# Kernel tuning notes

Measured on AMD Instinct MI355X. Metric: run time of the kernel, lower is better.

The kernel has to match this reference:

```python
import jax, jax.numpy as jnp
import numpy as np

B, V, D = 1024, 50000, 300
EPS = 1e-7


def setup_inputs() -> dict:
    key = jax.random.key(0)
    k1, k2 = jax.random.split(key)
    # soft multi-hot label mask over the vocab (torch code multiplies floats)
    labels = jax.random.uniform(k1, (B, V), dtype=jnp.float32)
    # pretrained word2vec-style embedding table
    weight = jax.random.normal(k2, (V, D), dtype=jnp.float32)
    return {"labels": labels, "weight": weight}


def reference(labels, weight):
    # torch: mul(weight, labels[:, :, None]).sum(1)  ==  labels @ weight
    attr = jnp.einsum('bv,vd->bd', labels, weight)  # (B, D)
    # L2 normalize: attr / (sqrt(sum(attr^2, 1)) + 1e-7)
    norm = jnp.sqrt(jnp.sum(attr * attr, axis=1, keepdims=True))
    return attr / (norm + EPS)
```

## Files before the change

kernel.cpp:

```cpp
#include <hip/hip_runtime.h>
#include <hip/hip_bf16.h>
#include <math.h>

typedef __bf16 bf16;
typedef bf16 bf16x8 __attribute__((ext_vector_type(8)));
typedef float f32x4 __attribute__((ext_vector_type(4)));

constexpr int Mdim = 1024;
constexpr int Kdim = 50000;
constexpr int Ndim = 300;
constexpr int NP   = 320;

constexpr int BM = 64, BN = 320, BK = 64;
constexpr int BKP = 72;
constexpr int MT = Mdim / BM;

__device__ __forceinline__ bf16x8 bzero8() {
    bf16x8 v;
#pragma unroll
    for (int e = 0; e < 8; ++e) v[e] = (bf16)0.0f;
    return v;
}

constexpr int TK = 64;
constexpr int TS = 301;
__global__ __launch_bounds__(256) void transpose_w(const float* __restrict__ W,
                                                   bf16* __restrict__ Wt)
{
    __shared__ bf16 tile[TK * TS];
    const int k0 = blockIdx.x * TK;
    const int t  = threadIdx.x;

    for (int c = t; c < 64 * 75; c += 256) {
        const int kk = c / 75;
        const int ch = c % 75;
        const int k  = k0 + kk;
        float4 v = make_float4(0.f, 0.f, 0.f, 0.f);
        if (k < Kdim) v = *(const float4*)(W + (size_t)k * Ndim + ch * 4);
        bf16* p = &tile[kk * TS + ch * 4];
        p[0] = (bf16)v.x; p[1] = (bf16)v.y; p[2] = (bf16)v.z; p[3] = (bf16)v.w;
    }
    __syncthreads();
    for (int c = t; c < NP * 8; c += 256) {
        const int n  = c >> 3;
        const int ch = c & 7;
        const int k  = k0 + ch * 8;
        if (k + 8 <= Kdim) {
            bf16x8 v = bzero8();
            if (n < Ndim) {
#pragma unroll
                for (int j = 0; j < 8; ++j) v[j] = tile[(ch * 8 + j) * TS + n];
            }
            *(bf16x8*)(Wt + (size_t)n * Kdim + k) = v;
        }
    }
}

template<int SPLIT, int SEGLEN, bool ATOMIC>
__global__ __launch_bounds__(512, 4) void gemm_kernel(const float* __restrict__ A,
                                                      const bf16* __restrict__ Wt,
                                                      float* __restrict__ out)
{
    __shared__ bf16 As[BM * BKP];
    __shared__ bf16 Bs[BN * BKP];

    const int bx   = blockIdx.x;
    const int mt   = bx & (MT - 1);
    const int ks   = bx >> 4;
    const int m0   = mt * BM;
    const int kbeg = ks * SEGLEN;
    const int kend = min(kbeg + SEGLEN, Kdim);

    const int t    = threadIdx.x;
    const int lane = t & 63;
    const int wave = t >> 6;
    const int wm   = wave >> 2;
    const int wn   = wave & 3;
    const int lm   = lane & 15;
    const int lq   = lane >> 4;

    const int arow = t >> 3;
    const int acol = (t & 7) * 8;
    const float* aptr = A + (size_t)(m0 + arow) * Kdim;

    float4 af[2];
    bf16x8 bfr[5];

    auto load_tiles = [&](int k0) {
        const int k = k0 + acol;
        if (k + 8 <= kend) {
            af[0] = *(const float4*)(aptr + k);
            af[1] = *(const float4*)(aptr + k + 4);
        } else {
            af[0] = make_float4(0.f, 0.f, 0.f, 0.f);
            af[1] = make_float4(0.f, 0.f, 0.f, 0.f);
        }
#pragma unroll
        for (int i = 0; i < 5; ++i) {
            const int c = t + 512 * i;
            const int brow = c >> 3;
            const int bcol = (c & 7) * 8;
            const int kk = k0 + bcol;
            bfr[i] = (kk + 8 <= kend) ? *(const bf16x8*)(Wt + (size_t)brow * Kdim + kk)
                                      : bzero8();
        }
    };
    auto store_tiles = [&]() {
        bf16x8 v;
        v[0]=(bf16)af[0].x; v[1]=(bf16)af[0].y; v[2]=(bf16)af[0].z; v[3]=(bf16)af[0].w;
        v[4]=(bf16)af[1].x; v[5]=(bf16)af[1].y; v[6]=(bf16)af[1].z; v[7]=(bf16)af[1].w;
        *(bf16x8*)(&As[arow * BKP + acol]) = v;
#pragma unroll
        for (int i = 0; i < 5; ++i) {
            const int c = t + 512 * i;
            const int brow = c >> 3;
            const int bcol = (c & 7) * 8;
            *(bf16x8*)(&Bs[brow * BKP + bcol]) = bfr[i];
        }
    };

    f32x4 acc[2][5] = {};

    load_tiles(kbeg);
    for (int k0 = kbeg; k0 < kend; k0 += BK) {
        store_tiles();
        __syncthreads();
        if (k0 + BK < kend) load_tiles(k0 + BK);
#pragma unroll
        for (int s = 0; s < 2; ++s) {
            bf16x8 a[2], b[5];
#pragma unroll
            for (int i = 0; i < 2; ++i)
                a[i] = *(const bf16x8*)(&As[(wm * 32 + i * 16 + lm) * BKP + s * 32 + lq * 8]);
#pragma unroll
            for (int j = 0; j < 5; ++j)
                b[j] = *(const bf16x8*)(&Bs[(wn * 80 + j * 16 + lm) * BKP + s * 32 + lq * 8]);
#pragma unroll
            for (int i = 0; i < 2; ++i)
#pragma unroll
                for (int j = 0; j < 5; ++j)
                    acc[i][j] = __builtin_amdgcn_mfma_f32_16x16x32_bf16(a[i], b[j], acc[i][j], 0, 0, 0);
        }
        __syncthreads();
    }

    const int col0 = wn * 80 + lm;
    const int rloc = wm * 32 + lq * 4;
    if (ATOMIC) {
#pragma unroll
        for (int i = 0; i < 2; ++i)
#pragma unroll
            for (int j = 0; j < 5; ++j)
#pragma unroll
                for (int r = 0; r < 4; ++r)
                    atomicAdd(&out[(size_t)(m0 + rloc + i * 16 + r) * NP + col0 + j * 16],
                              acc[i][j][r]);
    } else {
        float* P = out + (size_t)ks * Mdim * NP;
#pragma unroll
        for (int i = 0; i < 2; ++i)
#pragma unroll
            for (int j = 0; j < 5; ++j)
#pragma unroll
                for (int r = 0; r < 4; ++r)
                    P[(size_t)(m0 + rloc + i * 16 + r) * NP + col0 + j * 16] = acc[i][j][r];
    }
}

__global__ __launch_bounds__(320) void reduce_norm_k(const float* __restrict__ P,
                                                     float* __restrict__ out,
                                                     int split)
{
    const int b = blockIdx.x;
    const int t = threadIdx.x;
    float v = 0.f;
    for (int ks = 0; ks < split; ++ks)
        v += P[((size_t)ks * Mdim + b) * NP + t];
    float ss = v * v;
#pragma unroll
    for (int o = 32; o > 0; o >>= 1) ss += __shfl_down(ss, o, 64);
    __shared__ float wsum[5];
    __shared__ float scale;
    if ((t & 63) == 0) wsum[t >> 6] = ss;
    __syncthreads();
    if (t == 0) {
        float s = wsum[0] + wsum[1] + wsum[2] + wsum[3] + wsum[4];
        scale = 1.0f / (sqrtf(s) + 1e-7f);
    }
    __syncthreads();
    if (t < Ndim) out[(size_t)b * Ndim + t] = v * scale;
}

__global__ __launch_bounds__(320) void normalize_k(const float* __restrict__ Cacc,
                                                   float* __restrict__ out)
{
    const int b = blockIdx.x;
    const int t = threadIdx.x;
    float v = 0.f;
    if (t < Ndim) v = Cacc[(size_t)b * NP + t];
    float ss = v * v;
#pragma unroll
    for (int o = 32; o > 0; o >>= 1) ss += __shfl_down(ss, o, 64);
    __shared__ float wsum[5];
    __shared__ float scale;
    if ((t & 63) == 0) wsum[t >> 6] = ss;
    __syncthreads();
    if (t == 0) {
        float s = wsum[0] + wsum[1] + wsum[2] + wsum[3] + wsum[4];
        scale = 1.0f / (sqrtf(s) + 1e-7f);
    }
    __syncthreads();
    if (t < Ndim) out[(size_t)b * Ndim + t] = v * scale;
}

extern "C" void kernel_launch(void* const* d_in, const int* in_sizes, int n_in,
                              void* d_out, int out_size, void* d_ws, size_t ws_size,
                              hipStream_t stream)
{
    const float* labels = (const float*)d_in[0];
    const float* weight = (const float*)d_in[1];
    float* out = (float*)d_out;

    bf16* Wt = (bf16*)d_ws;
    const size_t wtBytes  = (size_t)NP * Kdim * sizeof(bf16);
    float* aux = (float*)((char*)d_ws + wtBytes);
    const size_t perSplit = (size_t)Mdim * NP * sizeof(float);

    transpose_w<<<dim3((Kdim + TK - 1) / TK), dim3(256), 0, stream>>>(weight, Wt);

    if (ws_size >= wtBytes + 32 * perSplit) {
        gemm_kernel<32, 1600, false><<<dim3(MT * 32), dim3(512), 0, stream>>>(labels, Wt, aux);
        reduce_norm_k<<<dim3(Mdim), dim3(320), 0, stream>>>(aux, out, 32);
    } else if (ws_size >= wtBytes + 16 * perSplit) {
        gemm_kernel<16, 3136, false><<<dim3(MT * 16), dim3(512), 0, stream>>>(labels, Wt, aux);
        reduce_norm_k<<<dim3(Mdim), dim3(320), 0, stream>>>(aux, out, 16);
    } else {
        hipMemsetAsync(aux, 0, perSplit, stream);
        gemm_kernel<32, 1600, true><<<dim3(MT * 32), dim3(512), 0, stream>>>(labels, Wt, aux);
        normalize_k<<<dim3(Mdim), dim3(320), 0, stream>>>(aux, out);
    }
}
```

Before: 381.3 us.

## Double-buffer LDS tiles with BK=32 and one barrier per k-step

The GEMM main loop now uses two LDS buffers and a K tile of 32 instead of one buffer with a K tile of 64. The next tile is stored into the alternate buffer after the MFMAs, which removes one __syncthreads per iteration and overlaps the LDS writes with compute. Global loads shrink to 16-byte float4 for A and 8-byte uint2 for B, and row/column indices are precomputed. The cost is narrower global loads, twice as many loop iterations, and more barriers per unit of K, while total LDS use stays about the same.

Result: slower. 413.0 us (+8.3%).

```diff
diff --git a/kernel.cpp b/kernel.cpp
--- a/kernel.cpp
+++ b/kernel.cpp
@@ -4,6 +4,7 @@
 
 typedef __bf16 bf16;
 typedef bf16 bf16x8 __attribute__((ext_vector_type(8)));
+typedef bf16 bf16x4 __attribute__((ext_vector_type(4)));
 typedef float f32x4 __attribute__((ext_vector_type(4)));
 
 constexpr int Mdim = 1024;
@@ -11,16 +12,9 @@
 constexpr int Ndim = 300;
 constexpr int NP   = 320;
 
-constexpr int BM = 64, BN = 320, BK = 64;
-constexpr int BKP = 72;
+constexpr int BM = 64, BN = 320, BK = 32;
+constexpr int BKP = 40;
 constexpr int MT = Mdim / BM;
-
-__device__ __forceinline__ bf16x8 bzero8() {
-    bf16x8 v;
-#pragma unroll
-    for (int e = 0; e < 8; ++e) v[e] = (bf16)0.0f;
-    return v;
-}
 
 constexpr int TK = 64;
 constexpr int TS = 301;
@@ -46,7 +40,9 @@
         const int ch = c & 7;
         const int k  = k0 + ch * 8;
         if (k + 8 <= Kdim) {
-            bf16x8 v = bzero8();
+            bf16x8 v;
+#pragma unroll
+            for (int e = 0; e < 8; ++e) v[e] = (bf16)0.0f;
             if (n < Ndim) {
 #pragma unroll
                 for (int j = 0; j < 8; ++j) v[j] = tile[(ch * 8 + j) * TS + n];
@@ -61,8 +57,8 @@
                                                       const bf16* __restrict__ Wt,
                                                       float* __restrict__ out)
 {
-    __shared__ bf16 As[BM * BKP];
-    __shared__ bf16 Bs[BN * BKP];
+    __shared__ bf16 As[2][BM * BKP];
+    __shared__ bf16 Bs[2][BN * BKP];
 
     const int bx   = blockIdx.x;
     const int mt   = bx & (MT - 1);
@@ -80,68 +76,65 @@
     const int lq   = lane >> 4;
 
     const int arow = t >> 3;
-    const int acol = (t & 7) * 8;
-    const float* aptr = A + (size_t)(m0 + arow) * Kdim;
-
-    float4 af[2];
-    bf16x8 bfr[5];
+    const int acol = (t & 7) * 4;
+    const float* aptr = A + (size_t)(m0 + arow) * Kdim + acol;
+
+    int brow[5], bcol[5];
+#pragma unroll
+    for (int i = 0; i < 5; ++i) {
+        const int c = t + 512 * i;
+        brow[i] = c >> 3;
+        bcol[i] = (c & 7) * 4;
+    }
+
+    float4 af;
+    uint2  bfr[5];
 
     auto load_tiles = [&](int k0) {
-        const int k = k0 + acol;
-        if (k + 8 <= kend) {
-            af[0] = *(const float4*)(aptr + k);
-            af[1] = *(const float4*)(aptr + k + 4);
-        } else {
-            af[0] = make_float4(0.f, 0.f, 0.f, 0.f);
-            af[1] = make_float4(0.f, 0.f, 0.f, 0.f);
-        }
+        af = (k0 + acol + 4 <= kend) ? *(const float4*)(aptr + k0)
+                                     : make_float4(0.f, 0.f, 0.f, 0.f);
 #pragma unroll
         for (int i = 0; i < 5; ++i) {
-            const int c = t + 512 * i;
-            const int brow = c >> 3;
-            const int bcol = (c & 7) * 8;
-            const int kk = k0 + bcol;
-            bfr[i] = (kk + 8 <= kend) ? *(const bf16x8*)(Wt + (size_t)brow * Kdim + kk)
-                                      : bzero8();
+            const int kk = k0 + bcol[i];
+            bfr[i] = (kk + 4 <= kend)
+                   ? *(const uint2*)(Wt + (size_t)brow[i] * Kdim + kk)
+                   : make_uint2(0u, 0u);
         }
     };
-    auto store_tiles = [&]() {
-        bf16x8 v;
-        v[0]=(bf16)af[0].x; v[1]=(bf16)af[0].y; v[2]=(bf16)af[0].z; v[3]=(bf16)af[0].w;
-        v[4]=(bf16)af[1].x; v[5]=(bf16)af[1].y; v[6]=(bf16)af[1].z; v[7]=(bf16)af[1].w;
-        *(bf16x8*)(&As[arow * BKP + acol]) = v;
-#pragma unroll
-        for (int i = 0; i < 5; ++i) {
-            const int c = t + 512 * i;
-            const int brow = c >> 3;
-            const int bcol = (c & 7) * 8;
-            *(bf16x8*)(&Bs[brow * BKP + bcol]) = bfr[i];
-        }
+    auto store_tiles = [&](int buf) {
+        bf16x4 v;
+        v[0] = (bf16)af.x; v[1] = (bf16)af.y; v[2] = (bf16)af.z; v[3] = (bf16)af.w;
+        *(bf16x4*)(&As[buf][arow * BKP + acol]) = v;
+#pragma unroll
+        for (int i = 0; i < 5; ++i)
+            *(uint2*)(&Bs[buf][brow[i] * BKP + bcol[i]]) = bfr[i];
     };
 
     f32x4 acc[2][5] = {};
 
     load_tiles(kbeg);
+    store_tiles(0);
+    __syncthreads();
+
+    int cur = 0;
     for (int k0 = kbeg; k0 < kend; k0 += BK) {
-        store_tiles();
+        const bool more = (k0 + BK < kend);
+        if (more) load_tiles(k0 + BK);
+        bf16x8 a[2], b[5];
+#pragma unroll
+        for (int i = 0; i < 2; ++i)
+            a[i] = *(const bf16x8*)(&As[cur][(wm * 32 + i * 16 + lm) * BKP + lq * 8]);
+#pragma unroll
+        for (int j = 0; j < 5; ++j)
+            b[j] = *(const bf16x8*)(&Bs[cur][(wn * 80 + j * 16 + lm) * BKP + lq * 8]);
+#pragma unroll
+        for (int i = 0; i < 2; ++i)
+#pragma unroll
+            for (int j = 0; j < 5; ++j)
+                acc[i][j] = __builtin_amdgcn_mfma_f32_16x16x32_bf16(a[i], b[j], acc[i][j], 0, 0, 0);
+        if (more) store_tiles(cur ^ 1);
         __syncthreads();
-        if (k0 + BK < kend) load_tiles(k0 + BK);
-#pragma unroll
-        for (int s = 0; s < 2; ++s) {
-            bf16x8 a[2], b[5];
-#pragma unroll
-            for (int i = 0; i < 2; ++i)
-                a[i] = *(const bf16x8*)(&As[(wm * 32 + i * 16 + lm) * BKP + s * 32 + lq * 8]);
-#pragma unroll
-            for (int j = 0; j < 5; ++j)
-                b[j] = *(const bf16x8*)(&Bs[(wn * 80 + j * 16 + lm) * BKP + s * 32 + lq * 8]);
-#pragma unroll
-            for (int i = 0; i < 2; ++i)
-#pragma unroll
-                for (int j = 0; j < 5; ++j)
-                    acc[i][j] = __builtin_amdgcn_mfma_f32_16x16x32_bf16(a[i], b[j], acc[i][j], 0, 0, 0);
-        }
-        __syncthreads();
+        cur ^= 1;
     }
 
     const int col0 = wn * 80 + lm;
```

## Drop shared-memory staging; load MFMA fragments directly from global memory

Applied to the files above, without the earlier changes.

The GEMM kernel no longer stages A and B tiles through LDS with block-wide barriers. Each wave loads its MFMA operand fragments straight from global memory into registers, with a two-stage register double buffer for A and per-step B loads. This removes the LDS stores and loads and the syncthreads, but operand reuse across waves now has to come from L1/L2 instead of LDS. Each 64-byte A row chunk is also read by the four wn waves, and B by the two wm waves, so global traffic rises and the access pattern is strided.

After: 499.5 us. 1.31x slower.

```diff
diff --git a/kernel.cpp b/kernel.cpp
--- a/kernel.cpp
+++ b/kernel.cpp
@@ -11,14 +11,19 @@
 constexpr int Ndim = 300;
 constexpr int NP   = 320;
 
-constexpr int BM = 64, BN = 320, BK = 64;
-constexpr int BKP = 72;
+constexpr int BM = 64, BN = 320;
 constexpr int MT = Mdim / BM;
 
 __device__ __forceinline__ bf16x8 bzero8() {
     bf16x8 v;
 #pragma unroll
     for (int e = 0; e < 8; ++e) v[e] = (bf16)0.0f;
+    return v;
+}
+__device__ __forceinline__ f32x4 fzero4() {
+    f32x4 v;
+#pragma unroll
+    for (int e = 0; e < 4; ++e) v[e] = 0.0f;
     return v;
 }
 
@@ -61,15 +66,13 @@
                                                       const bf16* __restrict__ Wt,
                                                       float* __restrict__ out)
 {
-    __shared__ bf16 As[BM * BKP];
-    __shared__ bf16 Bs[BN * BKP];
-
     const int bx   = blockIdx.x;
     const int mt   = bx & (MT - 1);
     const int ks   = bx >> 4;
     const int m0   = mt * BM;
     const int kbeg = ks * SEGLEN;
     const int kend = min(kbeg + SEGLEN, Kdim);
+    const int klen = kend - kbeg;
 
     const int t    = threadIdx.x;
     const int lane = t & 63;
@@ -79,69 +82,68 @@
     const int lm   = lane & 15;
     const int lq   = lane >> 4;
 
-    const int arow = t >> 3;
-    const int acol = (t & 7) * 8;
-    const float* aptr = A + (size_t)(m0 + arow) * Kdim;
-
-    float4 af[2];
-    bf16x8 bfr[5];
-
-    auto load_tiles = [&](int k0) {
-        const int k = k0 + acol;
-        if (k + 8 <= kend) {
-            af[0] = *(const float4*)(aptr + k);
-            af[1] = *(const float4*)(aptr + k + 4);
+    const float* Ab = A  + (size_t)kbeg + lq * 8;
+    const bf16*  Bb = Wt + (size_t)kbeg + lq * 8;
+    unsigned aoff[2], boff[5];
+#pragma unroll
+    for (int i = 0; i < 2; ++i)
+        aoff[i] = (unsigned)((m0 + wm * 32 + i * 16 + lm) * Kdim);
+#pragma unroll
+    for (int j = 0; j < 5; ++j)
+        boff[j] = (unsigned)((wn * 80 + j * 16 + lm) * Kdim);
+
+    const int lk = lq * 8;
+
+    f32x4  acc[2][5] = {};
+    f32x4  a0[2][2], a1[2][2];
+    bf16x8 b[5];
+
+    auto loadA = [&](f32x4 dst[2][2], int koff) {
+        if (lk + koff + 8 <= klen) {
+#pragma unroll
+            for (int i = 0; i < 2; ++i) {
+                dst[i][0] = *(const f32x4*)(Ab + aoff[i] + koff);
+                dst[i][1] = *(const f32x4*)(Ab + aoff[i] + koff + 4);
+            }
         } else {
-            af[0] = make_float4(0.f, 0.f, 0.f, 0.f);
-            af[1] = make_float4(0.f, 0.f, 0.f, 0.f);
-        }
-#pragma unroll
-        for (int i = 0; i < 5; ++i) {
-            const int c = t + 512 * i;
-            const int brow = c >> 3;
-            const int bcol = (c & 7) * 8;
-            const int kk = k0 + bcol;
-            bfr[i] = (kk + 8 <= kend) ? *(const bf16x8*)(Wt + (size_t)brow * Kdim + kk)
-                                      : bzero8();
+#pragma unroll
+            for (int i = 0; i < 2; ++i) { dst[i][0] = fzero4(); dst[i][1] = fzero4(); }
         }
     };
-    auto store_tiles = [&]() {
-        bf16x8 v;
-        v[0]=(bf16)af[0].x; v[1]=(bf16)af[0].y; v[2]=(bf16)af[0].z; v[3]=(bf16)af[0].w;
-        v[4]=(bf16)af[1].x; v[5]=(bf16)af[1].y; v[6]=(bf16)af[1].z; v[7]=(bf16)af[1].w;
-        *(bf16x8*)(&As[arow * BKP + acol]) = v;
-#pragma unroll
-        for (int i = 0; i < 5; ++i) {
-            const int c = t + 512 * i;
-            const int brow = c >> 3;
-            const int bcol = (c & 7) * 8;
-            *(bf16x8*)(&Bs[brow * BKP + bcol]) = bfr[i];
+    auto loadB = [&](int koff) {
+        const bool ok = (lk + koff + 8 <= klen);
+#pragma unroll
+        for (int j = 0; j < 5; ++j)
+            b[j] = ok ? *(const bf16x8*)(Bb + boff[j] + koff) : bzero8();
+    };
+    auto compute = [&](const f32x4 a[2][2]) {
+        bf16x8 af[2];
+#pragma unroll
+        for (int i = 0; i < 2; ++i)
+#pragma unroll
+            for (int e = 0; e < 4; ++e) {
+                af[i][e]     = (bf16)a[i][0][e];
+                af[i][4 + e] = (bf16)a[i][1][e];
+            }
+#pragma unroll
+        for (int i = 0; i < 2; ++i)
+#pragma unroll
+            for (int j = 0; j < 5; ++j)
+                acc[i][j] = __builtin_amdgcn_mfma_f32_16x16x32_bf16(af[i], b[j], acc[i][j], 0, 0, 0);
+    };
+
+    const int nst = (klen + 31) / 32;
+
+    loadA(a0, 0);
+    for (int ts = 0; ts < nst; ts += 2) {
+        loadB(ts * 32);
+        if (ts + 1 < nst) loadA(a1, (ts + 1) * 32);
+        compute(a0);
+        if (ts + 1 < nst) {
+            loadB((ts + 1) * 32);
+            if (ts + 2 < nst) loadA(a0, (ts + 2) * 32);
+            compute(a1);
         }
-    };
-
-    f32x4 acc[2][5] = {};
-
-    load_tiles(kbeg);
-    for (int k0 = kbeg; k0 < kend; k0 += BK) {
-        store_tiles();
-        __syncthreads();
-        if (k0 + BK < kend) load_tiles(k0 + BK);
-#pragma unroll
-        for (int s = 0; s < 2; ++s) {
-            bf16x8 a[2], b[5];
-#pragma unroll
-            for (int i = 0; i < 2; ++i)
-                a[i] = *(const bf16x8*)(&As[(wm * 32 + i * 16 + lm) * BKP + s * 32 + lq * 8]);
-#pragma unroll
-            for (int j = 0; j < 5; ++j)
-                b[j] = *(const bf16x8*)(&Bs[(wn * 80 + j * 16 + lm) * BKP + s * 32 + lq * 8]);
-#pragma unroll
-            for (int i = 0; i < 2; ++i)
-#pragma unroll
-                for (int j = 0; j < 5; ++j)
-                    acc[i][j] = __builtin_amdgcn_mfma_f32_16x16x32_bf16(a[i], b[j], acc[i][j], 0, 0, 0);
-        }
-        __syncthreads();
     }
 
     const int col0 = wn * 80 + lm;
```
